# Optimization experiments

Hardware: AMD Instinct MI355X
Metric: run time of the kernel (lower is better)

## Reference

```python
import jax, jax.numpy as jnp
import numpy as np

D_MODEL = 256
NHEAD = 8
D_FF = 2 * D_MODEL
N_LAYERS = 4
LAYER_NAMES = ("self", "cross", "self", "cross")
EPS_ATTN = 1e-6
EPS_LN = 1e-5


def pos_encoding(x):
    # LoFTR-style 2D sinusoidal positional encoding, x: [N, C, H, W]
    n, c, h, w = x.shape
    d4 = c // 4
    # exp(arange(0, c//2, 2) * (-log(1e4) / (c//2)))
    div = jnp.exp(jnp.arange(d4, dtype=jnp.float32) * 2.0 * (-np.log(10000.0) / (c // 2)))
    xs = jnp.arange(w, dtype=jnp.float32)[None, None, :]   # [1,1,W]
    ys = jnp.arange(h, dtype=jnp.float32)[None, :, None]   # [1,H,1]
    dv = div[:, None, None]                                 # [d4,1,1]
    sx = jnp.broadcast_to(jnp.sin(xs * dv), (d4, h, w))
    cx = jnp.broadcast_to(jnp.cos(xs * dv), (d4, h, w))
    sy = jnp.broadcast_to(jnp.sin(ys * dv), (d4, h, w))
    cy = jnp.broadcast_to(jnp.cos(ys * dv), (d4, h, w))
    pe = jnp.stack([sx, cx, sy, cy], axis=1).reshape(c, h, w)  # channel order pe[0::4]=sin_x,...
    return x + pe[None]


def linear_attention(q, k, v):
    # q: [N,L,H,d], k/v: [N,S,H,d]
    Q = jax.nn.elu(q) + 1.0
    K = jax.nn.elu(k) + 1.0
    KV = jnp.einsum('nshd,nshm->nhmd', K, v)                 # [N,H,d,d]
    Z = 1.0 / (jnp.einsum('nlhd,nhd->nlh', Q, K.sum(axis=1)) + EPS_ATTN)
    return jnp.einsum('nlhd,nhmd,nlh->nlhm', Q, KV, Z)       # [N,L,H,d]


def layer_norm(x, g, b):
    m = jnp.mean(x, axis=-1, keepdims=True)
    v = jnp.mean(jnp.square(x - m), axis=-1, keepdims=True)
    return (x - m) / jnp.sqrt(v + EPS_LN) * g + b


def encoder_layer(x, src, p):
    N, L, _ = x.shape
    q = (x @ p['Wq'] + p['bq']).reshape(N, L, NHEAD, -1)
    S = src.shape[1]
    k = (src @ p['Wk'] + p['bk']).reshape(N, S, NHEAD, -1)
    v = (src @ p['Wv'] + p['bv']).reshape(N, S, NHEAD, -1)
    attn = linear_attention(q, k, v).reshape(N, L, -1) @ p['Wo'] + p['bo']
    x = layer_norm(x + attn, p['g1'], p['be1'])
    y = jax.nn.relu(x @ p['W1'] + p['b1']) @ p['W2'] + p['b2']
    return layer_norm(x + y, p['g2'], p['be2'])


def _params_at(i, Wq, bq, Wk, bk, Wv, bv, Wo, bo, W1, b1, W2, b2, g1, be1, g2, be2):
    return dict(Wq=Wq[i], bq=bq[i], Wk=Wk[i], bk=bk[i], Wv=Wv[i], bv=bv[i],
                Wo=Wo[i], bo=bo[i], W1=W1[i], b1=b1[i], W2=W2[i], b2=b2[i],
                g1=g1[i], be1=be1[i], g2=g2[i], be2=be2[i])


def setup_inputs() -> dict:
    key = jax.random.key(0)
    ks = jax.random.split(key, 16)
    N, C, H, W = 4, D_MODEL, 64, 64
    d, dff, Ln = D_MODEL, D_FF, N_LAYERS
    s = 1.0 / np.sqrt(d)
    sf = 1.0 / np.sqrt(dff)
    return {
        'ref_feature': jax.random.normal(ks[0], (N, C, H, W), jnp.float32),
        'src_feature': jax.random.normal(ks[1], (N, C, H, W), jnp.float32),
        'Wq': jax.random.normal(ks[2], (Ln, d, d), jnp.float32) * s,
        'bq': jnp.zeros((Ln, d), jnp.float32),
        'Wk': jax.random.normal(ks[3], (Ln, d, d), jnp.float32) * s,
        'bk': jnp.zeros((Ln, d), jnp.float32),
        'Wv': jax.random.normal(ks[4], (Ln, d, d), jnp.float32) * s,
        'bv': jnp.zeros((Ln, d), jnp.float32),
        'Wo': jax.random.normal(ks[5], (Ln, d, d), jnp.float32) * s,
        'bo': jnp.zeros((Ln, d), jnp.float32),
        'W1': jax.random.normal(ks[6], (Ln, d, dff), jnp.float32) * s,
        'b1': jnp.zeros((Ln, dff), jnp.float32),
        'W2': jax.random.normal(ks[7], (Ln, dff, d), jnp.float32) * sf,
        'b2': jnp.zeros((Ln, d), jnp.float32),
        'g1': jnp.ones((Ln, d), jnp.float32),
        'be1': jnp.zeros((Ln, d), jnp.float32),
        'g2': jnp.ones((Ln, d), jnp.float32),
        'be2': jnp.zeros((Ln, d), jnp.float32),
    }


def reference(ref_feature, src_feature, Wq, bq, Wk, bk, Wv, bv, Wo, bo,
              W1, b1, W2, b2, g1, be1, g2, be2):
    # FMT.forward(feat='cross')
    N, C, H, W = ref_feature.shape
    f0 = pos_encoding(ref_feature).transpose(0, 2, 3, 1).reshape(N, H * W, C)
    f1 = pos_encoding(src_feature).transpose(0, 2, 3, 1).reshape(N, H * W, C)
    p1 = jnp.concatenate([f0, f1], axis=0)   # [2N, L, C]
    p2 = jnp.concatenate([f1, f0], axis=0)
    for i, name in enumerate(LAYER_NAMES):
        p = _params_at(i, Wq, bq, Wk, bk, Wv, bv, Wo, bo, W1, b1, W2, b2, g1, be1, g2, be2)
        src = p1 if name == 'self' else p2
        p1 = encoder_layer(p1, src, p)
    out = p1.reshape(2 * N, H, W, C).transpose(0, 3, 1, 2)  # [2N, C, H, W]
    return out
```

## Files before the change

### kernel.cpp

```cpp
#include <hip/hip_runtime.h>
#include <hip/hip_bf16.h>

typedef __bf16 bf16;
typedef __attribute__((ext_vector_type(8))) __bf16 bf16x8;
typedef __attribute__((ext_vector_type(4))) __bf16 bf16x4;
typedef __attribute__((ext_vector_type(4))) float f32x4;

__device__ __forceinline__ bf16 f2bf(float f) { return (bf16)f; }

__device__ __forceinline__ void async_cp16(const void* g, void* l) {
    __builtin_amdgcn_global_load_lds(
        (const __attribute__((address_space(1))) unsigned int*)g,
        (__attribute__((address_space(3))) unsigned int*)l, 16, 0, 0);
}

__device__ __forceinline__ float pe_val(int c, int t) {
    int h = t >> 6, w = t & 63;
    int i = c >> 2, j = c & 3;
    float div = expf(-0.14391156831212787f * (float)i);
    float arg = ((j < 2) ? (float)w : (float)h) * div;
    return (j & 1) ? cosf(arg) : sinf(arg);
}

__global__ __launch_bounds__(1024) void encode_kernel(const float* __restrict__ ref,
                                                      const float* __restrict__ src,
                                                      bf16* __restrict__ Xb,
                                                      bf16* __restrict__ P2b) {
    __shared__ float tile[32][33];
    int n = blockIdx.z >> 1, sel = blockIdx.z & 1;
    const float* f = sel ? src : ref;
    int t = blockIdx.x * 32 + threadIdx.x;
    int c = blockIdx.y * 32 + threadIdx.y;
    float v = f[((size_t)n * 256 + c) * 4096 + t] + pe_val(c, t);
    tile[threadIdx.y][threadIdx.x] = v;
    __syncthreads();
    int tt = blockIdx.x * 32 + threadIdx.y;
    int cc = blockIdx.y * 32 + threadIdx.x;
    float o = tile[threadIdx.x][threadIdx.y];
    int bx = sel ? 4 + n : n;
    int bp = sel ? n : 4 + n;
    Xb [((size_t)bx * 4096 + tt) * 256 + cc] = f2bf(o);
    P2b[((size_t)bp * 4096 + tt) * 256 + cc] = f2bf(o);
}

__global__ __launch_bounds__(1024) void wt_conv(const float* __restrict__ Wq, const float* __restrict__ Wk,
                                                const float* __restrict__ Wv, const float* __restrict__ Wo,
                                                const float* __restrict__ W1, const float* __restrict__ W2,
                                                bf16* __restrict__ Wt) {
    __shared__ float t[32][33];
    int z = blockIdx.z, L = z / 6, m = z - L * 6;
    const float* src; int K, N, doff;
    if      (m == 0) { src = Wq + L * 65536;  K = 256; N = 256; doff = 0; }
    else if (m == 1) { src = Wk + L * 65536;  K = 256; N = 256; doff = 65536; }
    else if (m == 2) { src = Wv + L * 65536;  K = 256; N = 256; doff = 131072; }
    else if (m == 3) { src = Wo + L * 65536;  K = 256; N = 256; doff = 196608; }
    else if (m == 4) { src = W1 + L * 131072; K = 256; N = 512; doff = 262144; }
    else             { src = W2 + L * 131072; K = 512; N = 256; doff = 393216; }
    int n0 = blockIdx.x * 32, k0 = blockIdx.y * 32;
    if (n0 >= N || k0 >= K) return;
    t[threadIdx.y][threadIdx.x] = src[(size_t)(k0 + threadIdx.y) * N + n0 + threadIdx.x];
    __syncthreads();
    bf16* dst = Wt + (size_t)L * 524288 + doff;
    dst[(size_t)(n0 + threadIdx.y) * K + k0 + threadIdx.x] = f2bf(t[threadIdx.x][threadIdx.y]);
}

__global__ __launch_bounds__(256) void gemm_qkv(const bf16* __restrict__ Aq,
                                                const bf16* __restrict__ Akv,
                                                const bf16* __restrict__ Wt,
                                                const float* __restrict__ bq,
                                                const float* __restrict__ bk,
                                                const float* __restrict__ bv,
                                                bf16* __restrict__ Q,
                                                bf16* __restrict__ Ko,
                                                bf16* __restrict__ V) {
    __shared__ bf16 Als[128 * 64];
    __shared__ bf16 Bls[128 * 64];
    int tid = threadIdx.x;
    int wave = tid >> 6, lane = tid & 63;
    int bm = blockIdx.y * 128, bn = blockIdx.x * 128;
    int wm = (wave >> 1) * 64, wn = (wave & 1) * 64;
    int l15 = lane & 15, g = lane >> 4;
    const int K = 256;

    int seg = bn >> 8, cloc = bn & 255;
    const bf16* A = seg == 0 ? Aq : Akv;
    const float* bias = seg == 0 ? bq : (seg == 1 ? bk : bv);
    bf16* Out = seg == 0 ? Q : (seg == 1 ? Ko : V);
    bool do_elu = seg < 2;

    f32x4 acc[4][4] = {};

    for (int k0 = 0; k0 < K; k0 += 64) {
#pragma unroll
        for (int r = 0; r < 4; ++r) {
            int Lc = r * 256 + tid;
            int row = Lc >> 3, cs = Lc & 7;
            int gc = cs ^ (row & 7);
            async_cp16(A  + (size_t)(bm + row) * K + k0 + gc * 8, &Als[Lc * 8]);
            async_cp16(Wt + (size_t)(bn + row) * K + k0 + gc * 8, &Bls[Lc * 8]);
        }
        __syncthreads();
#pragma unroll
        for (int ks = 0; ks < 2; ++ks) {
            bf16x8 af[4], bfr[4];
#pragma unroll
            for (int i = 0; i < 4; ++i) {
                int row = wm + i * 16 + l15;
                int c = ks * 4 + g;
                af[i] = *(bf16x8*)&Als[row * 64 + ((c ^ (row & 7)) * 8)];
            }
#pragma unroll
            for (int j = 0; j < 4; ++j) {
                int row = wn + j * 16 + l15;
                int c = ks * 4 + g;
                bfr[j] = *(bf16x8*)&Bls[row * 64 + ((c ^ (row & 7)) * 8)];
            }
#pragma unroll
            for (int i = 0; i < 4; ++i)
#pragma unroll
                for (int j = 0; j < 4; ++j)
                    acc[i][j] = __builtin_amdgcn_mfma_f32_16x16x32_bf16(af[i], bfr[j], acc[i][j], 0, 0, 0);
        }
        __syncthreads();
    }

    int r4 = (lane >> 4) * 4;
#pragma unroll
    for (int i = 0; i < 4; ++i) {
#pragma unroll
        for (int j = 0; j < 4; ++j) {
            int cj = cloc + wn + j * 16 + l15;
            float bvv = bias[cj];
#pragma unroll
            for (int r = 0; r < 4; ++r) {
                int row = bm + wm + i * 16 + r4 + r;
                float v = acc[i][j][r] + bvv;
                if (do_elu) v = v > 0.f ? v + 1.f : expf(v);
                Out[(size_t)row * 256 + cj] = f2bf(v);
            }
        }
    }
}

template <int RELU>
__global__ __launch_bounds__(256) void gemm_mfma(const bf16* __restrict__ A,
                                                 const bf16* __restrict__ Wt,
                                                 const float* __restrict__ bias,
                                                 bf16* __restrict__ C,
                                                 int N, int K) {
    __shared__ bf16 Als[128 * 64];
    __shared__ bf16 Bls[128 * 64];
    int tid = threadIdx.x;
    int wave = tid >> 6, lane = tid & 63;
    int bm = blockIdx.y * 128, bn = blockIdx.x * 128;
    int wm = (wave >> 1) * 64, wn = (wave & 1) * 64;
    int l15 = lane & 15, g = lane >> 4;

    f32x4 acc[4][4] = {};

    for (int k0 = 0; k0 < K; k0 += 64) {
#pragma unroll
        for (int r = 0; r < 4; ++r) {
            int Lc = r * 256 + tid;
            int row = Lc >> 3, cs = Lc & 7;
            int gc = cs ^ (row & 7);
            async_cp16(A  + (size_t)(bm + row) * K + k0 + gc * 8, &Als[Lc * 8]);
            async_cp16(Wt + (size_t)(bn + row) * K + k0 + gc * 8, &Bls[Lc * 8]);
        }
        __syncthreads();
#pragma unroll
        for (int ks = 0; ks < 2; ++ks) {
            bf16x8 af[4], bfr[4];
#pragma unroll
            for (int i = 0; i < 4; ++i) {
                int row = wm + i * 16 + l15;
                int c = ks * 4 + g;
                af[i] = *(bf16x8*)&Als[row * 64 + ((c ^ (row & 7)) * 8)];
            }
#pragma unroll
            for (int j = 0; j < 4; ++j) {
                int row = wn + j * 16 + l15;
                int c = ks * 4 + g;
                bfr[j] = *(bf16x8*)&Bls[row * 64 + ((c ^ (row & 7)) * 8)];
            }
#pragma unroll
            for (int i = 0; i < 4; ++i)
#pragma unroll
                for (int j = 0; j < 4; ++j)
                    acc[i][j] = __builtin_amdgcn_mfma_f32_16x16x32_bf16(af[i], bfr[j], acc[i][j], 0, 0, 0);
        }
        __syncthreads();
    }

    int r4 = (lane >> 4) * 4;
#pragma unroll
    for (int i = 0; i < 4; ++i) {
#pragma unroll
        for (int j = 0; j < 4; ++j) {
            int col = bn + wn + j * 16 + l15;
            float bvv = bias[col];
#pragma unroll
            for (int r = 0; r < 4; ++r) {
                int row = bm + wm + i * 16 + r4 + r;
                float v = acc[i][j][r] + bvv;
                if (RELU) v = fmaxf(v, 0.f);
                C[(size_t)row * N + col] = f2bf(v);
            }
        }
    }
}

__global__ __launch_bounds__(512) void gemm_ln(const bf16* __restrict__ A,
                                               const bf16* __restrict__ Wt,
                                               const float* __restrict__ bias,
                                               bf16* __restrict__ Xb,
                                               const float* __restrict__ g,
                                               const float* __restrict__ b,
                                               int K) {
    __shared__ __align__(16) char smem[128 * 260 * 2];
    bf16* Als = (bf16*)smem;
    bf16* Bls = (bf16*)(smem + 16384);
    bf16* Cls = (bf16*)smem;

    int tid = threadIdx.x;
    int wave = tid >> 6, lane = tid & 63;
    int bm = blockIdx.x * 128;
    int wm = (wave >> 2) * 64, wn = (wave & 3) * 64;
    int l15 = lane & 15, gg = lane >> 4;

    f32x4 acc[4][4] = {};

    for (int k0 = 0; k0 < K; k0 += 64) {
#pragma unroll
        for (int r = 0; r < 2; ++r) {
            int Lc = r * 512 + tid;
            int row = Lc >> 3, cs = Lc & 7;
            int gc = cs ^ (row & 7);
            async_cp16(A + (size_t)(bm + row) * K + k0 + gc * 8, &Als[Lc * 8]);
        }
#pragma unroll
        for (int r = 0; r < 4; ++r) {
            int Lc = r * 512 + tid;
            int row = Lc >> 3, cs = Lc & 7;
            int gc = cs ^ (row & 7);
            async_cp16(Wt + (size_t)row * K + k0 + gc * 8, &Bls[Lc * 8]);
        }
        __syncthreads();
#pragma unroll
        for (int ks = 0; ks < 2; ++ks) {
            bf16x8 af[4], bfr[4];
#pragma unroll
            for (int i = 0; i < 4; ++i) {
                int row = wm + i * 16 + l15;
                int c = ks * 4 + gg;
                af[i] = *(bf16x8*)&Als[row * 64 + ((c ^ (row & 7)) * 8)];
            }
#pragma unroll
            for (int j = 0; j < 4; ++j) {
                int row = wn + j * 16 + l15;
                int c = ks * 4 + gg;
                bfr[j] = *(bf16x8*)&Bls[row * 64 + ((c ^ (row & 7)) * 8)];
            }
#pragma unroll
            for (int i = 0; i < 4; ++i)
#pragma unroll
                for (int j = 0; j < 4; ++j)
                    acc[i][j] = __builtin_amdgcn_mfma_f32_16x16x32_bf16(af[i], bfr[j], acc[i][j], 0, 0, 0);
        }
        __syncthreads();
    }

    int r4 = (lane >> 4) * 4;
#pragma unroll
    for (int j = 0; j < 4; ++j) {
        int col = wn + j * 16 + l15;
        float bvv = bias[col];
#pragma unroll
        for (int i = 0; i < 4; ++i)
#pragma unroll
            for (int r = 0; r < 4; ++r)
                Cls[(wm + i * 16 + r4 + r) * 260 + col] = f2bf(acc[i][j][r] + bvv);
    }
    __syncthreads();

    int c4 = lane * 4;
    float4 gw = *(const float4*)&g[c4];
    float4 bw = *(const float4*)&b[c4];
#pragma unroll 2
    for (int rw = 0; rw < 16; ++rw) {
        int row = wave * 16 + rw;
        size_t gidx = (size_t)(bm + row) * 256 + c4;
        bf16x4 xb = *(const bf16x4*)(Xb + gidx);
        bf16x4 cb = *(const bf16x4*)&Cls[row * 260 + c4];
        float4 v;
        v.x = (float)xb[0] + (float)cb[0];
        v.y = (float)xb[1] + (float)cb[1];
        v.z = (float)xb[2] + (float)cb[2];
        v.w = (float)xb[3] + (float)cb[3];
        float s  = v.x + v.y + v.z + v.w;
        float sq = v.x * v.x + v.y * v.y + v.z * v.z + v.w * v.w;
#pragma unroll
        for (int off = 32; off > 0; off >>= 1) {
            s  += __shfl_xor(s,  off);
            sq += __shfl_xor(sq, off);
        }
        float mean = s * (1.f / 256.f);
        float var  = sq * (1.f / 256.f) - mean * mean;
        float rstd = rsqrtf(var + 1e-5f);
        bf16x4 ob;
        ob[0] = f2bf((v.x - mean) * rstd * gw.x + bw.x);
        ob[1] = f2bf((v.y - mean) * rstd * gw.y + bw.y);
        ob[2] = f2bf((v.z - mean) * rstd * gw.z + bw.z);
        ob[3] = f2bf((v.w - mean) * rstd * gw.w + bw.w);
        *(bf16x4*)(Xb + gidx) = ob;
    }
}

__global__ __launch_bounds__(512) void attn_oln(const bf16* __restrict__ Qb,
                                                const float* __restrict__ KV,
                                                const float* __restrict__ Ksum,
                                                const bf16* __restrict__ Wt,
                                                const float* __restrict__ bias,
                                                bf16* __restrict__ Xb,
                                                const float* __restrict__ g,
                                                const float* __restrict__ b) {
    __shared__ __align__(16) char smem[132096];
    __shared__ float Zs[32][8];
    float* Qs  = (float*)smem;
    bf16*  Wls = (bf16*)smem;
    bf16*  Cls = (bf16*)smem;
    bf16*  Bt  = (bf16*)(smem + 66560);

    int tid = threadIdx.x;
    int r0 = blockIdx.x * 128;
    int n = r0 >> 12;

    int c = tid & 255, tg = tid >> 8;
    int h = c >> 5, m = c & 31;
    float kvr[32];
    const float* kvp = KV + (size_t)(n * 8 + h) * 1024 + m * 32;
#pragma unroll
    for (int q4 = 0; q4 < 8; ++q4) *(float4*)&kvr[q4 * 4] = *(const float4*)(kvp + q4 * 4);

    int col8 = (c >> 3) & 7, elem = c & 7, slice = c >> 6;

    for (int it = 0; it < 4; ++it) {
        int t0 = it * 32;
        const bf16* qsrc = Qb + (size_t)(r0 + t0) * 256;
#pragma unroll
        for (int kk = 0; kk < 2; ++kk) {
            int e8 = kk * 512 + tid;
            bf16x8 v = *(const bf16x8*)(qsrc + (size_t)e8 * 8);
            int t = e8 >> 5, c8 = e8 & 31;
#pragma unroll
            for (int u = 0; u < 8; ++u) Qs[t * 260 + c8 * 8 + u] = (float)v[u];
        }
        __syncthreads();
        if (tid < 256) {
            int tz = tid >> 3, hz = tid & 7;
            const float* ksp = Ksum + n * 256 + hz * 32;
            float z = 0.f;
#pragma unroll
            for (int q4 = 0; q4 < 8; ++q4) {
                float4 qv = *(float4*)&Qs[tz * 260 + hz * 32 + q4 * 4];
                float4 kq = *(const float4*)(ksp + q4 * 4);
                z += qv.x * kq.x + qv.y * kq.y + qv.z * kq.z + qv.w * kq.w;
            }
            Zs[tz][hz] = 1.f / (z + 1e-6f);
        }
        __syncthreads();
#pragma unroll 2
        for (int tt = 0; tt < 16; ++tt) {
            int t = tg * 16 + tt;
            float acc = 0.f;
#pragma unroll
            for (int q4 = 0; q4 < 8; ++q4) {
                float4 qv = *(float4*)&Qs[t * 260 + h * 32 + q4 * 4];
                acc += qv.x * kvr[q4 * 4 + 0] + qv.y * kvr[q4 * 4 + 1]
                     + qv.z * kvr[q4 * 4 + 2] + qv.w * kvr[q4 * 4 + 3];
            }
            int row = t0 + t;
            Bt[slice * 8192 + row * 64 + ((col8 ^ (row & 7)) * 8) + elem] =
                f2bf(acc * Zs[t][h]);
        }
        __syncthreads();
    }

    int wave = tid >> 6, lane = tid & 63;
    int wm = (wave >> 2) * 64, wn = (wave & 3) * 64;
    int l15 = lane & 15, gg = lane >> 4;
    f32x4 acc[4][4] = {};

    for (int k0 = 0; k0 < 256; k0 += 64) {
#pragma unroll
        for (int r = 0; r < 4; ++r) {
            int Lc = r * 512 + tid;
            int row = Lc >> 3, cs = Lc & 7;
            int gc = cs ^ (row & 7);
            async_cp16(Wt + (size_t)row * 256 + k0 + gc * 8, &Wls[Lc * 8]);
        }
        __syncthreads();
        const bf16* Asl = Bt + (k0 >> 6) * 8192;
#pragma unroll
        for (int ks = 0; ks < 2; ++ks) {
            bf16x8 af[4], bfr[4];
#pragma unroll
            for (int i = 0; i < 4; ++i) {
                int row = wm + i * 16 + l15;
                int cc = ks * 4 + gg;
                af[i] = *(bf16x8*)&Asl[row * 64 + ((cc ^ (row & 7)) * 8)];
            }
#pragma unroll
            for (int j = 0; j < 4; ++j) {
                int row = wn + j * 16 + l15;
                int cc = ks * 4 + gg;
                bfr[j] = *(bf16x8*)&Wls[row * 64 + ((cc ^ (row & 7)) * 8)];
            }
#pragma unroll
            for (int i = 0; i < 4; ++i)
#pragma unroll
                for (int j = 0; j < 4; ++j)
                    acc[i][j] = __builtin_amdgcn_mfma_f32_16x16x32_bf16(af[i], bfr[j], acc[i][j], 0, 0, 0);
        }
        __syncthreads();
    }

    int r4 = (lane >> 4) * 4;
#pragma unroll
    for (int j = 0; j < 4; ++j) {
        int col = wn + j * 16 + l15;
        float bvv = bias[col];
#pragma unroll
        for (int i = 0; i < 4; ++i)
#pragma unroll
            for (int r = 0; r < 4; ++r)
                Cls[(wm + i * 16 + r4 + r) * 260 + col] = f2bf(acc[i][j][r] + bvv);
    }
    __syncthreads();

    int c4 = lane * 4;
    float4 gw = *(const float4*)&g[c4];
    float4 bw = *(const float4*)&b[c4];
#pragma unroll 2
    for (int rw = 0; rw < 16; ++rw) {
        int row = wave * 16 + rw;
        size_t gidx = (size_t)(r0 + row) * 256 + c4;
        bf16x4 xb = *(const bf16x4*)(Xb + gidx);
        bf16x4 cb = *(const bf16x4*)&Cls[row * 260 + c4];
        float4 v;
        v.x = (float)xb[0] + (float)cb[0];
        v.y = (float)xb[1] + (float)cb[1];
        v.z = (float)xb[2] + (float)cb[2];
        v.w = (float)xb[3] + (float)cb[3];
        float s  = v.x + v.y + v.z + v.w;
        float sq = v.x * v.x + v.y * v.y + v.z * v.z + v.w * v.w;
#pragma unroll
        for (int off = 32; off > 0; off >>= 1) {
            s  += __shfl_xor(s,  off);
            sq += __shfl_xor(sq, off);
        }
        float mean = s * (1.f / 256.f);
        float var  = sq * (1.f / 256.f) - mean * mean;
        float rstd = rsqrtf(var + 1e-5f);
        bf16x4 ob;
        ob[0] = f2bf((v.x - mean) * rstd * gw.x + bw.x);
        ob[1] = f2bf((v.y - mean) * rstd * gw.y + bw.y);
        ob[2] = f2bf((v.z - mean) * rstd * gw.z + bw.z);
        ob[3] = f2bf((v.w - mean) * rstd * gw.w + bw.w);
        *(bf16x4*)(Xb + gidx) = ob;
    }
}

__global__ __launch_bounds__(256) void kv_prep_part(const bf16* __restrict__ Kb,
                                                    const bf16* __restrict__ Vb,
                                                    float* __restrict__ Pkv,
                                                    float* __restrict__ Pks) {
    __shared__ float Ks[128][32];
    __shared__ float Vs[128][32];
    int sp = blockIdx.x;
    int nh = blockIdx.y;
    int n = nh >> 3, h = nh & 7;
    int tid = threadIdx.x;
    int wave = tid >> 6, lane = tid & 63;
    int mg = lane >> 3;
    int dg = lane & 7;
    size_t base = ((size_t)n * 4096 + sp * 128) * 256 + h * 32;

#pragma unroll
    for (int p = 0; p < 2; ++p) {
        int r = p * 64 + (tid >> 2);
        int c = (tid & 3) * 8;
        bf16x8 k8 = *(const bf16x8*)(Kb + base + (size_t)r * 256 + c);
        bf16x8 v8 = *(const bf16x8*)(Vb + base + (size_t)r * 256 + c);
#pragma unroll
        for (int u = 0; u < 8; ++u) { Ks[r][c + u] = (float)k8[u]; Vs[r][c + u] = (float)v8[u]; }
    }
    __syncthreads();

    float acc[4][4] = {};
    float ks4[4] = {};
    int s0 = wave * 32;
    for (int s = s0; s < s0 + 32; ++s) {
        float4 kq = *(float4*)&Ks[s][dg * 4];
        float4 vq = *(float4*)&Vs[s][mg * 4];
        ks4[0] += kq.x; ks4[1] += kq.y; ks4[2] += kq.z; ks4[3] += kq.w;
        acc[0][0] += vq.x * kq.x; acc[0][1] += vq.x * kq.y; acc[0][2] += vq.x * kq.z; acc[0][3] += vq.x * kq.w;
        acc[1][0] += vq.y * kq.x; acc[1][1] += vq.y * kq.y; acc[1][2] += vq.y * kq.z; acc[1][3] += vq.y * kq.w;
        acc[2][0] += vq.z * kq.x; acc[2][1] += vq.z * kq.y; acc[2][2] += vq.z * kq.z; acc[2][3] += vq.z * kq.w;
        acc[3][0] += vq.w * kq.x; acc[3][1] += vq.w * kq.y; acc[3][2] += vq.w * kq.z; acc[3][3] += vq.w * kq.w;
    }
    __syncthreads();

    float* R  = &Ks[0][0];
    float* RS = &Vs[0][0];
#pragma unroll
    for (int mi = 0; mi < 4; ++mi)
#pragma unroll
        for (int dj = 0; dj < 4; ++dj)
            R[wave * 1024 + (mg * 4 + mi) * 32 + dg * 4 + dj] = acc[mi][dj];
    if (mg == 0)
#pragma unroll
        for (int dj = 0; dj < 4; ++dj) RS[wave * 32 + dg * 4 + dj] = ks4[dj];
    __syncthreads();

    int e = tid * 4;
    float4 o0 = *(float4*)&R[e];
    float4 o1 = *(float4*)&R[1024 + e];
    float4 o2 = *(float4*)&R[2048 + e];
    float4 o3 = *(float4*)&R[3072 + e];
    float4 o = make_float4(o0.x + o1.x + o2.x + o3.x, o0.y + o1.y + o2.y + o3.y,
                           o0.z + o1.z + o2.z + o3.z, o0.w + o1.w + o2.w + o3.w);
    *(float4*)&Pkv[((size_t)nh * 32 + sp) * 1024 + e] = o;
    if (tid < 32)
        Pks[((size_t)nh * 32 + sp) * 32 + tid] = RS[tid] + RS[32 + tid] + RS[64 + tid] + RS[96 + tid];
}

__global__ __launch_bounds__(64) void kv_reduce(const float* __restrict__ Pkv,
                                                const float* __restrict__ Pks,
                                                float* __restrict__ KV,
                                                float* __restrict__ Ksum) {
    int nh = blockIdx.x;
    int q = blockIdx.y;
    int e = (q * 64 + threadIdx.x) * 4;
    float4 s = make_float4(0.f, 0.f, 0.f, 0.f);
    for (int sp = 0; sp < 32; ++sp) {
        float4 p = *(const float4*)&Pkv[((size_t)nh * 32 + sp) * 1024 + e];
        s.x += p.x; s.y += p.y; s.z += p.z; s.w += p.w;
    }
    *(float4*)&KV[(size_t)nh * 1024 + e] = s;
    if (q == 0 && threadIdx.x < 32) {
        float ss = 0.f;
        for (int sp = 0; sp < 32; ++sp) ss += Pks[((size_t)nh * 32 + sp) * 32 + threadIdx.x];
        Ksum[nh * 32 + threadIdx.x] = ss;
    }
}

__global__ __launch_bounds__(1024) void store_kernel(const bf16* __restrict__ Xb,
                                                     float* __restrict__ out) {
    __shared__ float tile[32][33];
    int b = blockIdx.z;
    int t0 = blockIdx.x * 32, c0 = blockIdx.y * 32;
    tile[threadIdx.y][threadIdx.x] =
        (float)Xb[((size_t)b * 4096 + t0 + threadIdx.y) * 256 + c0 + threadIdx.x];
    __syncthreads();
    out[((size_t)b * 256 + c0 + threadIdx.y) * 4096 + t0 + threadIdx.x] =
        tile[threadIdx.x][threadIdx.y];
}

extern "C" void kernel_launch(void* const* d_in, const int* in_sizes, int n_in,
                              void* d_out, int out_size, void* d_ws, size_t ws_size,
                              hipStream_t stream) {
    const float* ref  = (const float*)d_in[0];
    const float* srcf = (const float*)d_in[1];
    const float* Wq = (const float*)d_in[2];
    const float* bq = (const float*)d_in[3];
    const float* Wk = (const float*)d_in[4];
    const float* bk = (const float*)d_in[5];
    const float* Wv = (const float*)d_in[6];
    const float* bv = (const float*)d_in[7];
    const float* Wo = (const float*)d_in[8];
    const float* bo = (const float*)d_in[9];
    const float* W1 = (const float*)d_in[10];
    const float* b1 = (const float*)d_in[11];
    const float* W2 = (const float*)d_in[12];
    const float* b2 = (const float*)d_in[13];
    const float* g1 = (const float*)d_in[14];
    const float* be1 = (const float*)d_in[15];
    const float* g2 = (const float*)d_in[16];
    const float* be2 = (const float*)d_in[17];

    const size_t SZ = (size_t)8 * 4096 * 256;
    float* ws  = (float*)d_ws;
    float* KVb = ws;
    float* Ksb = KVb + 65536;
    float* Pkv = Ksb + 2048;
    float* Pks = Pkv + 2097152;
    bf16*  Wt  = (bf16*)(Pks + 65536);
    bf16*  Xb  = Wt + 2097152;
    bf16*  P2b = Xb + SZ;
    bf16*  Qb  = P2b + SZ;
    bf16*  Kb  = (bf16*)d_out;
    bf16*  Vb  = Kb + SZ;
    bf16*  Hb  = Kb;

    wt_conv<<<dim3(16, 16, 24), dim3(32, 32), 0, stream>>>(Wq, Wk, Wv, Wo, W1, W2, Wt);
    encode_kernel<<<dim3(128, 8, 8), dim3(32, 32), 0, stream>>>(ref, srcf, Xb, P2b);

    for (int L = 0; L < 4; ++L) {
        const bf16* WtL = Wt + (size_t)L * 524288;
        const bf16* Akv = (L & 1) ? P2b : Xb;
        gemm_qkv<<<dim3(6, 256), 256, 0, stream>>>(Xb, Akv, WtL,
                                                   bq + L * 256, bk + L * 256, bv + L * 256,
                                                   Qb, Kb, Vb);
        kv_prep_part<<<dim3(32, 64), 256, 0, stream>>>(Kb, Vb, Pkv, Pks);
        kv_reduce<<<dim3(64, 4), 64, 0, stream>>>(Pkv, Pks, KVb, Ksb);
        attn_oln<<<256, 512, 0, stream>>>(Qb, KVb, Ksb, WtL + 196608, bo + L * 256,
                                          Xb, g1 + L * 256, be1 + L * 256);
        gemm_mfma<1><<<dim3(4, 256), 256, 0, stream>>>(Xb, WtL + 262144, b1 + L * 512, Hb, 512, 256);
        gemm_ln<<<256, 512, 0, stream>>>(Hb, WtL + 393216, b2 + L * 256, Xb,
                                         g2 + L * 256, be2 + L * 256, 512);
    }

    store_kernel<<<dim3(128, 8, 8), dim3(32, 32), 0, stream>>>(Xb, (float*)d_out);
}
```

Baseline: 673.9 us.

## Halve attn_oln row tile and read Wo fragments directly from global

The attention-output+LayerNorm kernel now processes 64 rows per block instead of 128 and launches twice as many blocks. Shared memory shrinks from about 132KB to about 50KB, so more blocks can be resident per CU and more CUs have work. The Wo tile is no longer staged in LDS via async copies. Each wave loads its B fragments straight from global memory, which removes per-k-step barriers but relies on cache hits for the repeated weight reads.

```diff
diff --git a/kernel.cpp b/kernel.cpp
--- a/kernel.cpp
+++ b/kernel.cpp
@@ -324,15 +324,14 @@
                                                 bf16* __restrict__ Xb,
                                                 const float* __restrict__ g,
                                                 const float* __restrict__ b) {
-    __shared__ __align__(16) char smem[132096];
-    __shared__ float Zs[32][8];
+    __shared__ __align__(16) char smem[49920];
     float* Qs  = (float*)smem;
-    bf16*  Wls = (bf16*)smem;
+    float* Zs  = (float*)(smem + 16640);
+    bf16*  Bt  = (bf16*)(smem + 17152);
     bf16*  Cls = (bf16*)smem;
-    bf16*  Bt  = (bf16*)(smem + 66560);
 
     int tid = threadIdx.x;
-    int r0 = blockIdx.x * 128;
+    int r0 = blockIdx.x * 64;
     int n = r0 >> 12;
 
     int c = tid & 255, tg = tid >> 8;
@@ -345,18 +344,16 @@
     int col8 = (c >> 3) & 7, elem = c & 7, slice = c >> 6;
 
     for (int it = 0; it < 4; ++it) {
-        int t0 = it * 32;
+        int t0 = it * 16;
         const bf16* qsrc = Qb + (size_t)(r0 + t0) * 256;
-#pragma unroll
-        for (int kk = 0; kk < 2; ++kk) {
-            int e8 = kk * 512 + tid;
-            bf16x8 v = *(const bf16x8*)(qsrc + (size_t)e8 * 8);
-            int t = e8 >> 5, c8 = e8 & 31;
+        {
+            int t = tid >> 5, c8 = tid & 31;
+            bf16x8 v = *(const bf16x8*)(qsrc + (size_t)tid * 8);
 #pragma unroll
             for (int u = 0; u < 8; ++u) Qs[t * 260 + c8 * 8 + u] = (float)v[u];
         }
         __syncthreads();
-        if (tid < 256) {
+        if (tid < 128) {
             int tz = tid >> 3, hz = tid & 7;
             const float* ksp = Ksum + n * 256 + hz * 32;
             float z = 0.f;
@@ -366,12 +363,12 @@
                 float4 kq = *(const float4*)(ksp + q4 * 4);
                 z += qv.x * kq.x + qv.y * kq.y + qv.z * kq.z + qv.w * kq.w;
             }
-            Zs[tz][hz] = 1.f / (z + 1e-6f);
+            Zs[tz * 8 + hz] = 1.f / (z + 1e-6f);
         }
         __syncthreads();
 #pragma unroll 2
-        for (int tt = 0; tt < 16; ++tt) {
-            int t = tg * 16 + tt;
+        for (int tt = 0; tt < 8; ++tt) {
+            int t = tg * 8 + tt;
             float acc = 0.f;
 #pragma unroll
             for (int q4 = 0; q4 < 8; ++q4) {
@@ -380,32 +377,24 @@
                      + qv.z * kvr[q4 * 4 + 2] + qv.w * kvr[q4 * 4 + 3];
             }
             int row = t0 + t;
-            Bt[slice * 8192 + row * 64 + ((col8 ^ (row & 7)) * 8) + elem] =
-                f2bf(acc * Zs[t][h]);
+            Bt[slice * 4096 + row * 64 + ((col8 ^ (row & 7)) * 8) + elem] =
+                f2bf(acc * Zs[t * 8 + h]);
         }
         __syncthreads();
     }
 
     int wave = tid >> 6, lane = tid & 63;
-    int wm = (wave >> 2) * 64, wn = (wave & 3) * 64;
+    int wm = (wave >> 2) * 32, wn = (wave & 3) * 64;
     int l15 = lane & 15, gg = lane >> 4;
-    f32x4 acc[4][4] = {};
+    f32x4 acc2[2][4] = {};
 
     for (int k0 = 0; k0 < 256; k0 += 64) {
-#pragma unroll
-        for (int r = 0; r < 4; ++r) {
-            int Lc = r * 512 + tid;
-            int row = Lc >> 3, cs = Lc & 7;
-            int gc = cs ^ (row & 7);
-            async_cp16(Wt + (size_t)row * 256 + k0 + gc * 8, &Wls[Lc * 8]);
-        }
-        __syncthreads();
-        const bf16* Asl = Bt + (k0 >> 6) * 8192;
+        const bf16* Asl = Bt + (k0 >> 6) * 4096;
 #pragma unroll
         for (int ks = 0; ks < 2; ++ks) {
-            bf16x8 af[4], bfr[4];
-#pragma unroll
-            for (int i = 0; i < 4; ++i) {
+            bf16x8 af[2], bfr[4];
+#pragma unroll
+            for (int i = 0; i < 2; ++i) {
                 int row = wm + i * 16 + l15;
                 int cc = ks * 4 + gg;
                 af[i] = *(bf16x8*)&Asl[row * 64 + ((cc ^ (row & 7)) * 8)];
@@ -413,17 +402,16 @@
 #pragma unroll
             for (int j = 0; j < 4; ++j) {
                 int row = wn + j * 16 + l15;
-                int cc = ks * 4 + gg;
-                bfr[j] = *(bf16x8*)&Wls[row * 64 + ((cc ^ (row & 7)) * 8)];
-            }
-#pragma unroll
-            for (int i = 0; i < 4; ++i)
+                bfr[j] = *(const bf16x8*)(Wt + (size_t)row * 256 + k0 + ks * 32 + gg * 8);
+            }
+#pragma unroll
+            for (int i = 0; i < 2; ++i)
 #pragma unroll
                 for (int j = 0; j < 4; ++j)
-                    acc[i][j] = __builtin_amdgcn_mfma_f32_16x16x32_bf16(af[i], bfr[j], acc[i][j], 0, 0, 0);
-        }
-        __syncthreads();
-    }
+                    acc2[i][j] = __builtin_amdgcn_mfma_f32_16x16x32_bf16(af[i], bfr[j], acc2[i][j], 0, 0, 0);
+        }
+    }
+    __syncthreads();
 
     int r4 = (lane >> 4) * 4;
 #pragma unroll
@@ -431,10 +419,10 @@
         int col = wn + j * 16 + l15;
         float bvv = bias[col];
 #pragma unroll
-        for (int i = 0; i < 4; ++i)
+        for (int i = 0; i < 2; ++i)
 #pragma unroll
             for (int r = 0; r < 4; ++r)
-                Cls[(wm + i * 16 + r4 + r) * 260 + col] = f2bf(acc[i][j][r] + bvv);
+                Cls[(wm + i * 16 + r4 + r) * 260 + col] = f2bf(acc2[i][j][r] + bvv);
     }
     __syncthreads();
 
@@ -442,8 +430,8 @@
     float4 gw = *(const float4*)&g[c4];
     float4 bw = *(const float4*)&b[c4];
 #pragma unroll 2
-    for (int rw = 0; rw < 16; ++rw) {
-        int row = wave * 16 + rw;
+    for (int rw = 0; rw < 8; ++rw) {
+        int row = wave * 8 + rw;
         size_t gidx = (size_t)(r0 + row) * 256 + c4;
         bf16x4 xb = *(const bf16x4*)(Xb + gidx);
         bf16x4 cb = *(const bf16x4*)&Cls[row * 260 + c4];
@@ -614,7 +602,7 @@
                                                    Qb, Kb, Vb);
         kv_prep_part<<<dim3(32, 64), 256, 0, stream>>>(Kb, Vb, Pkv, Pks);
         kv_reduce<<<dim3(64, 4), 64, 0, stream>>>(Pkv, Pks, KVb, Ksb);
-        attn_oln<<<256, 512, 0, stream>>>(Qb, KVb, Ksb, WtL + 196608, bo + L * 256,
+        attn_oln<<<512, 512, 0, stream>>>(Qb, KVb, Ksb, WtL + 196608, bo + L * 256,
                                           Xb, g1 + L * 256, be1 + L * 256);
         gemm_mfma<1><<<dim3(4, 256), 256, 0, stream>>>(Xb, WtL + 262144, b1 + L * 512, Hb, 512, 256);
         gemm_ln<<<256, 512, 0, stream>>>(Hb, WtL + 393216, b2 + L * 256, Xb,
```

New measurement: 745.5 us. 10.6% more time.

## Fold per-batch KV into output projection weights, replacing per-row attention matmul

Applied to the files above, without the earlier changes.

Instead of computing Q·KV per token and then multiplying by Wo, a new weff_kernel precomputes per-batch effective weights (KV folded into Wo) and a zcalc kernel computes per-row-per-head normalizers. The fused GEMM+LayerNorm kernel then scales Q by Z while loading it into LDS and runs a single MFMA GEMM against the effective weights. This removes the scalar fp32 per-token attention stage, at the cost of two extra launches, a small weight-fold computation per batch, and an extra bf16 rounding of the folded weights.

```diff
diff --git a/kernel.cpp b/kernel.cpp
--- a/kernel.cpp
+++ b/kernel.cpp
@@ -316,79 +316,25 @@
     }
 }
 
-__global__ __launch_bounds__(512) void attn_oln(const bf16* __restrict__ Qb,
-                                                const float* __restrict__ KV,
-                                                const float* __restrict__ Ksum,
-                                                const bf16* __restrict__ Wt,
-                                                const float* __restrict__ bias,
-                                                bf16* __restrict__ Xb,
-                                                const float* __restrict__ g,
-                                                const float* __restrict__ b) {
-    __shared__ __align__(16) char smem[132096];
-    __shared__ float Zs[32][8];
-    float* Qs  = (float*)smem;
-    bf16*  Wls = (bf16*)smem;
-    bf16*  Cls = (bf16*)smem;
-    bf16*  Bt  = (bf16*)(smem + 66560);
+__global__ __launch_bounds__(512) void gemm_attn_ln(const bf16* __restrict__ A,
+                                                    const float* __restrict__ Zt,
+                                                    const bf16* __restrict__ Weff,
+                                                    const float* __restrict__ bias,
+                                                    bf16* __restrict__ Xb,
+                                                    const float* __restrict__ g,
+                                                    const float* __restrict__ b) {
+    __shared__ __align__(16) char smem[128 * 260 * 2];
+    bf16* Als = (bf16*)smem;
+    bf16* Bls = (bf16*)(smem + 16384);
+    bf16* Cls = (bf16*)smem;
 
     int tid = threadIdx.x;
-    int r0 = blockIdx.x * 128;
-    int n = r0 >> 12;
-
-    int c = tid & 255, tg = tid >> 8;
-    int h = c >> 5, m = c & 31;
-    float kvr[32];
-    const float* kvp = KV + (size_t)(n * 8 + h) * 1024 + m * 32;
-#pragma unroll
-    for (int q4 = 0; q4 < 8; ++q4) *(float4*)&kvr[q4 * 4] = *(const float4*)(kvp + q4 * 4);
-
-    int col8 = (c >> 3) & 7, elem = c & 7, slice = c >> 6;
-
-    for (int it = 0; it < 4; ++it) {
-        int t0 = it * 32;
-        const bf16* qsrc = Qb + (size_t)(r0 + t0) * 256;
-#pragma unroll
-        for (int kk = 0; kk < 2; ++kk) {
-            int e8 = kk * 512 + tid;
-            bf16x8 v = *(const bf16x8*)(qsrc + (size_t)e8 * 8);
-            int t = e8 >> 5, c8 = e8 & 31;
-#pragma unroll
-            for (int u = 0; u < 8; ++u) Qs[t * 260 + c8 * 8 + u] = (float)v[u];
-        }
-        __syncthreads();
-        if (tid < 256) {
-            int tz = tid >> 3, hz = tid & 7;
-            const float* ksp = Ksum + n * 256 + hz * 32;
-            float z = 0.f;
-#pragma unroll
-            for (int q4 = 0; q4 < 8; ++q4) {
-                float4 qv = *(float4*)&Qs[tz * 260 + hz * 32 + q4 * 4];
-                float4 kq = *(const float4*)(ksp + q4 * 4);
-                z += qv.x * kq.x + qv.y * kq.y + qv.z * kq.z + qv.w * kq.w;
-            }
-            Zs[tz][hz] = 1.f / (z + 1e-6f);
-        }
-        __syncthreads();
-#pragma unroll 2
-        for (int tt = 0; tt < 16; ++tt) {
-            int t = tg * 16 + tt;
-            float acc = 0.f;
-#pragma unroll
-            for (int q4 = 0; q4 < 8; ++q4) {
-                float4 qv = *(float4*)&Qs[t * 260 + h * 32 + q4 * 4];
-                acc += qv.x * kvr[q4 * 4 + 0] + qv.y * kvr[q4 * 4 + 1]
-                     + qv.z * kvr[q4 * 4 + 2] + qv.w * kvr[q4 * 4 + 3];
-            }
-            int row = t0 + t;
-            Bt[slice * 8192 + row * 64 + ((col8 ^ (row & 7)) * 8) + elem] =
-                f2bf(acc * Zs[t][h]);
-        }
-        __syncthreads();
-    }
-
     int wave = tid >> 6, lane = tid & 63;
+    int bm = blockIdx.x * 128;
+    const bf16* Wt = Weff + (size_t)(bm >> 12) * 65536;
     int wm = (wave >> 2) * 64, wn = (wave & 3) * 64;
     int l15 = lane & 15, gg = lane >> 4;
+
     f32x4 acc[4][4] = {};
 
     for (int k0 = 0; k0 < 256; k0 += 64) {
@@ -397,24 +343,36 @@
             int Lc = r * 512 + tid;
             int row = Lc >> 3, cs = Lc & 7;
             int gc = cs ^ (row & 7);
-            async_cp16(Wt + (size_t)row * 256 + k0 + gc * 8, &Wls[Lc * 8]);
-        }
-        __syncthreads();
-        const bf16* Asl = Bt + (k0 >> 6) * 8192;
+            async_cp16(Wt + (size_t)row * 256 + k0 + gc * 8, &Bls[Lc * 8]);
+        }
+#pragma unroll
+        for (int r = 0; r < 2; ++r) {
+            int Lc = r * 512 + tid;
+            int row = Lc >> 3, cs = Lc & 7;
+            int gc = cs ^ (row & 7);
+            int gcol = k0 + gc * 8;
+            bf16x8 q8 = *(const bf16x8*)(A + (size_t)(bm + row) * 256 + gcol);
+            float z = Zt[(size_t)(bm + row) * 8 + (gcol >> 5)];
+            bf16x8 a8;
+#pragma unroll
+            for (int u = 0; u < 8; ++u) a8[u] = f2bf((float)q8[u] * z);
+            *(bf16x8*)&Als[Lc * 8] = a8;
+        }
+        __syncthreads();
 #pragma unroll
         for (int ks = 0; ks < 2; ++ks) {
             bf16x8 af[4], bfr[4];
 #pragma unroll
             for (int i = 0; i < 4; ++i) {
                 int row = wm + i * 16 + l15;
-                int cc = ks * 4 + gg;
-                af[i] = *(bf16x8*)&Asl[row * 64 + ((cc ^ (row & 7)) * 8)];
+                int c = ks * 4 + gg;
+                af[i] = *(bf16x8*)&Als[row * 64 + ((c ^ (row & 7)) * 8)];
             }
 #pragma unroll
             for (int j = 0; j < 4; ++j) {
                 int row = wn + j * 16 + l15;
-                int cc = ks * 4 + gg;
-                bfr[j] = *(bf16x8*)&Wls[row * 64 + ((cc ^ (row & 7)) * 8)];
+                int c = ks * 4 + gg;
+                bfr[j] = *(bf16x8*)&Bls[row * 64 + ((c ^ (row & 7)) * 8)];
             }
 #pragma unroll
             for (int i = 0; i < 4; ++i)
@@ -444,7 +402,7 @@
 #pragma unroll 2
     for (int rw = 0; rw < 16; ++rw) {
         int row = wave * 16 + rw;
-        size_t gidx = (size_t)(r0 + row) * 256 + c4;
+        size_t gidx = (size_t)(bm + row) * 256 + c4;
         bf16x4 xb = *(const bf16x4*)(Xb + gidx);
         bf16x4 cb = *(const bf16x4*)&Cls[row * 260 + c4];
         float4 v;
@@ -553,6 +511,69 @@
         for (int sp = 0; sp < 32; ++sp) ss += Pks[((size_t)nh * 32 + sp) * 32 + threadIdx.x];
         Ksum[nh * 32 + threadIdx.x] = ss;
     }
+}
+
+__global__ __launch_bounds__(256) void weff_kernel(const float* __restrict__ KV,
+                                                   const bf16* __restrict__ WtO,
+                                                   bf16* __restrict__ Weff) {
+    __shared__ float KVs[8][1024];
+    int n = blockIdx.y, c0 = blockIdx.x * 64;
+    int tid = threadIdx.x;
+    const float* src = KV + (size_t)n * 8192;
+    for (int i = tid; i < 2048; i += 256)
+        *(float4*)&((float*)KVs)[i * 4] = *(const float4*)&src[i * 4];
+    __syncthreads();
+
+    int c = c0 + (tid & 63);
+    int hb = tid >> 6;
+    const bf16* wrow = WtO + (size_t)c * 256 + hb * 64;
+    bf16* dst = Weff + (size_t)n * 65536 + (size_t)c * 256 + hb * 64;
+
+#pragma unroll
+    for (int hh = 0; hh < 2; ++hh) {
+        int h = hb * 2 + hh;
+        float wo[32];
+#pragma unroll
+        for (int u = 0; u < 4; ++u) {
+            bf16x8 w8 = *(const bf16x8*)(wrow + hh * 32 + u * 8);
+#pragma unroll
+            for (int v = 0; v < 8; ++v) wo[u * 8 + v] = (float)w8[v];
+        }
+        float s[32] = {};
+        for (int m = 0; m < 32; ++m) {
+            float wm = wo[m];
+#pragma unroll
+            for (int d4 = 0; d4 < 8; ++d4) {
+                float4 kv4 = *(float4*)&KVs[h][m * 32 + d4 * 4];
+                s[d4 * 4 + 0] += wm * kv4.x;
+                s[d4 * 4 + 1] += wm * kv4.y;
+                s[d4 * 4 + 2] += wm * kv4.z;
+                s[d4 * 4 + 3] += wm * kv4.w;
+            }
+        }
+#pragma unroll
+        for (int u = 0; u < 4; ++u) {
+            bf16x8 o8;
+#pragma unroll
+            for (int v = 0; v < 8; ++v) o8[v] = f2bf(s[u * 8 + v]);
+            *(bf16x8*)(dst + hh * 32 + u * 8) = o8;
+        }
+    }
+}
+
+__global__ __launch_bounds__(256) void zcalc(const bf16* __restrict__ Qb,
+                                             const float* __restrict__ Ksum,
+                                             float* __restrict__ Zt) {
+    int row = blockIdx.x * 4 + (threadIdx.x >> 6);
+    int lane = threadIdx.x & 63;
+    int n = row >> 12;
+    int c = lane * 4;
+    bf16x4 q = *(const bf16x4*)(Qb + (size_t)row * 256 + c);
+    float4 k = *(const float4*)&Ksum[n * 256 + c];
+    float s = (float)q[0] * k.x + (float)q[1] * k.y + (float)q[2] * k.z + (float)q[3] * k.w;
+    s += __shfl_xor(s, 1); s += __shfl_xor(s, 2); s += __shfl_xor(s, 4);
+    if ((lane & 7) == 0)
+        Zt[(size_t)row * 8 + (lane >> 3)] = 1.f / (s + 1e-6f);
 }
 
 __global__ __launch_bounds__(1024) void store_kernel(const bf16* __restrict__ Xb,
@@ -599,6 +620,8 @@
     bf16*  Xb  = Wt + 2097152;
     bf16*  P2b = Xb + SZ;
     bf16*  Qb  = P2b + SZ;
+    bf16*  Weffb = (bf16*)Pkv;
+    float* Ztb   = Pkv + 262144;
     bf16*  Kb  = (bf16*)d_out;
     bf16*  Vb  = Kb + SZ;
     bf16*  Hb  = Kb;
@@ -614,8 +637,10 @@
                                                    Qb, Kb, Vb);
         kv_prep_part<<<dim3(32, 64), 256, 0, stream>>>(Kb, Vb, Pkv, Pks);
         kv_reduce<<<dim3(64, 4), 64, 0, stream>>>(Pkv, Pks, KVb, Ksb);
-        attn_oln<<<256, 512, 0, stream>>>(Qb, KVb, Ksb, WtL + 196608, bo + L * 256,
-                                          Xb, g1 + L * 256, be1 + L * 256);
+        weff_kernel<<<dim3(4, 8), 256, 0, stream>>>(KVb, WtL + 196608, Weffb);
+        zcalc<<<8192, 256, 0, stream>>>(Qb, Ksb, Ztb);
+        gemm_attn_ln<<<256, 512, 0, stream>>>(Qb, Ztb, Weffb, bo + L * 256, Xb,
+                                              g1 + L * 256, be1 + L * 256);
         gemm_mfma<1><<<dim3(4, 256), 256, 0, stream>>>(Xb, WtL + 262144, b1 + L * 512, Hb, 512, 256);
         gemm_ln<<<256, 512, 0, stream>>>(Hb, WtL + 393216, b2 + L * 256, Xb,
                                          g2 + L * 256, be2 + L * 256, 512);
```

Measured after the change: 683.6 us. Within noise of the previous version (+1.4%).
